# Performance work log

Hardware: AMD Instinct MI355X
Metric: run time of the kernel (lower is better)

## Reference

```python
import jax, jax.numpy as jnp
import numpy as np

B, M, H, D, C = 512, 40, 128, 64, 128


def setup_inputs() -> dict:
    key = jax.random.key(0)
    k1, k2, k3, k4 = jax.random.split(key, 4)
    x0 = jax.random.normal(k1, (B, M, D), dtype=jnp.float32)
    xk = jax.random.normal(k2, (B, H, D), dtype=jnp.float32)
    # Conv1d(kernel_size=1) weight [C, H*M, 1] squeezed to [C, H*M]; bias [C]
    W = jax.random.normal(k3, (C, H * M), dtype=jnp.float32) * 0.02
    b = jax.random.normal(k4, (C,), dtype=jnp.float32) * 0.02
    return {"x0": x0, "xk": xk, "W": W, "b": b}


def reference(x0, xk, W, b):
    # torch: outer[b, h*M+m, d] = xk[b,h,d] * x0[b,m,d]; out = conv1d(outer)
    # conv1d with kernel_size=1 is a channel contraction:
    #   out[b,c,d] = sum_{h,m} W[c, h*M+m] * xk[b,h,d] * x0[b,m,d] + b[c]
    Bsz, Hh, Dd = xk.shape
    Mm = x0.shape[1]
    Cc = W.shape[0]
    Wr = W.reshape(Cc, Hh, Mm)  # channel index is h*M + m -> [C, H, M]
    out = jnp.einsum('bhd,bmd,chm->bcd', xk, x0, Wr) + b[None, :, None]
    return out  # [B, C, D]
```

## Files before the change

kernel.cpp:

```cpp
#include <hip/hip_runtime.h>
#include <hip/hip_bf16.h>

typedef __attribute__((ext_vector_type(8))) short short8;
typedef __attribute__((ext_vector_type(4))) float f32x4;
typedef unsigned short u16;
typedef unsigned int u32;

#define NB 512
#define NM 40
#define NH 128
#define ND 64
#define NC 128
#define KTOT 5120

__device__ __forceinline__ u16 f2bf_rne(float f) {
    u32 u = __float_as_uint(f);
    u32 r = u + 0x7FFFu + ((u >> 16) & 1u);
    return (u16)(r >> 16);
}

__global__ void w3_kernel(const float* __restrict__ W, u16* __restrict__ W3) {
    __shared__ u16 kbuf[NH * 20];
    const int c = blockIdx.x >> 1, mh = blockIdx.x & 1;
    const float* src = W + (size_t)c * KTOT + mh * 20;
    for (int i = threadIdx.x; i < NH * 5; i += 256) {
        int h = i / 5, j4 = i % 5;
        float4 v = *(const float4*)(src + h * NM + j4 * 4);
        u16* kb = kbuf + h * 20 + j4 * 4;
        kb[0] = f2bf_rne(v.x); kb[1] = f2bf_rne(v.y);
        kb[2] = f2bf_rne(v.z); kb[3] = f2bf_rne(v.w);
    }
    __syncthreads();
    for (int i = threadIdx.x; i < 320; i += 256) {
        int mo = i >> 4, t = (i >> 2) & 3, q = i & 3;
        int n = (mh * 20 + mo) * 16 + t * 4 + q;
        union { short8 s8; u16 e[8]; } v;
#pragma unroll
        for (int j = 0; j < 8; ++j)
            v.e[j] = kbuf[(t * 32 + q * 8 + j) * 20 + mo];
        *(short8*)(W3 + ((size_t)n * 128 + c) * 8) = v.s8;
    }
}

__global__ void __launch_bounds__(512, 4) cin_main(
    const float* __restrict__ x0g, const float* __restrict__ xkg,
    const float* __restrict__ biasg, const u16* __restrict__ W3,
    float* __restrict__ out)
{
    __shared__ __align__(16) char smem[29824];
    short* xkT    = (short*)smem;
    float* x0s    = (float*)(smem + 18432);
    float* bias_s = (float*)(smem + 29312);

    const int tid = threadIdx.x;
    const int w = tid >> 6, L = tid & 63;
    const int q = L >> 4, l16 = L & 15;
    const int rh = w;
    const size_t b = blockIdx.x;

    const u16* Ap = W3 + q * 1024 + (size_t)(rh * 16 + l16) * 8;

    short8 aP[2];
    aP[0] = *(const short8*)(Ap + 0 * 4096);
    aP[1] = *(const short8*)(Ap + 1 * 4096);

    for (int i = tid; i < 2048; i += 512) {
        int h = i >> 4, d4 = (i & 15) << 2;
        float4 v = *(const float4*)(xkg + b * (NH * ND) + h * ND + d4);
        xkT[(d4 + 0) * 144 + h] = (short)f2bf_rne(v.x);
        xkT[(d4 + 1) * 144 + h] = (short)f2bf_rne(v.y);
        xkT[(d4 + 2) * 144 + h] = (short)f2bf_rne(v.z);
        xkT[(d4 + 3) * 144 + h] = (short)f2bf_rne(v.w);
    }
    for (int i = tid; i < 640; i += 512) {
        int m = i >> 4, d4 = (i & 15) << 2;
        *(f32x4*)(x0s + m * 68 + d4) =
            *(const f32x4*)(x0g + b * (NM * ND) + m * ND + d4);
    }
    if (tid < NC) bias_s[tid] = biasg[tid];
    __syncthreads();

    const short* Bp = xkT + (size_t)l16 * 144 + q * 8;
    short8 bR[4][4];
#pragma unroll
    for (int t = 0; t < 4; ++t)
#pragma unroll
        for (int n = 0; n < 4; ++n)
            bR[t][n] = *(const short8*)(Bp + n * (16 * 144) + t * 32);

    float s[4], sn[4];
#pragma unroll
    for (int n = 0; n < 4; ++n)
        s[n] = x0s[n * 16 + l16];

    f32x4 T[4] = {{0.f,0.f,0.f,0.f},{0.f,0.f,0.f,0.f},{0.f,0.f,0.f,0.f},{0.f,0.f,0.f,0.f}};
    f32x4 o[4] = {{0.f,0.f,0.f,0.f},{0.f,0.f,0.f,0.f},{0.f,0.f,0.f,0.f},{0.f,0.f,0.f,0.f}};

#pragma unroll 4
    for (int u = 0; u < 160; ++u) {
        const int t = u & 3;
        const short8 a = aP[u & 1];
        const int up = (u + 2 < 160) ? (u + 2) : 159;
        aP[u & 1] = *(const short8*)(Ap + (size_t)up * 4096);
        if (t == 0) {
            const int m = u >> 2;
#pragma unroll
            for (int n = 0; n < 4; ++n)
                sn[n] = (m < 39) ? x0s[(m + 1) * 68 + n * 16 + l16] : 0.f;
        }
        T[0] = __builtin_amdgcn_mfma_f32_16x16x32_bf16(a, bR[t][0], T[0], 0, 0, 0);
        T[1] = __builtin_amdgcn_mfma_f32_16x16x32_bf16(a, bR[t][1], T[1], 0, 0, 0);
        T[2] = __builtin_amdgcn_mfma_f32_16x16x32_bf16(a, bR[t][2], T[2], 0, 0, 0);
        T[3] = __builtin_amdgcn_mfma_f32_16x16x32_bf16(a, bR[t][3], T[3], 0, 0, 0);
        if (t == 3) {
#pragma unroll
            for (int n = 0; n < 4; ++n) {
                const float dd = s[n] - sn[n];
                o[n] += dd * T[n];
                s[n] = sn[n];
            }
        }
    }

    float* op = out + b * (NC * ND);
#pragma unroll
    for (int n = 0; n < 4; ++n) {
        const int d = n * 16 + l16;
#pragma unroll
        for (int rr = 0; rr < 4; ++rr) {
            const int c = rh * 16 + q * 4 + rr;
            op[c * ND + d] = o[n][rr] + bias_s[c];
        }
    }
}

extern "C" void kernel_launch(void* const* d_in, const int* in_sizes, int n_in,
                              void* d_out, int out_size, void* d_ws, size_t ws_size,
                              hipStream_t stream) {
    const float* x0 = (const float*)d_in[0];
    const float* xk = (const float*)d_in[1];
    const float* W  = (const float*)d_in[2];
    const float* bi = (const float*)d_in[3];
    float* out = (float*)d_out;

    u16* W3 = (u16*)d_ws;

    w3_kernel<<<NC * 2, 256, 0, stream>>>(W, W3);
    cin_main<<<NB, 512, 0, stream>>>(x0, xk, bi, W3, out);
}
```

Baseline: 116.4 us.

## Split output channels across blocks, split K across waves, stage W via LDS ring

```diff
diff --git a/kernel.cpp b/kernel.cpp
--- a/kernel.cpp
+++ b/kernel.cpp
@@ -17,6 +17,12 @@
     u32 u = __float_as_uint(f);
     u32 r = u + 0x7FFFu + ((u >> 16) & 1u);
     return (u16)(r >> 16);
+}
+
+__device__ __forceinline__ void gload16(const void* g, void* l) {
+    __builtin_amdgcn_global_load_lds(
+        (const __attribute__((address_space(1))) void*)g,
+        (__attribute__((address_space(3))) void*)l, 16, 0, 0);
 }
 
 __global__ void w3_kernel(const float* __restrict__ W, u16* __restrict__ W3) {
@@ -47,22 +53,30 @@
     const float* __restrict__ biasg, const u16* __restrict__ W3,
     float* __restrict__ out)
 {
-    __shared__ __align__(16) char smem[29824];
-    short* xkT    = (short*)smem;
-    float* x0s    = (float*)(smem + 18432);
-    float* bias_s = (float*)(smem + 29312);
+    __shared__ __align__(16) char smem[62592];
+    char*  ring   = smem;
+    float* red    = (float*)smem;
+    short* xkT    = (short*)(smem + 32768);
+    float* x0s    = (float*)(smem + 51200);
+    float* bias_s = (float*)(smem + 62080);
 
     const int tid = threadIdx.x;
     const int w = tid >> 6, L = tid & 63;
     const int q = L >> 4, l16 = L & 15;
-    const int rh = w;
-    const size_t b = blockIdx.x;
+    const int kh = w & 1;
+    const int rh = w >> 1;
+    const int ch = blockIdx.x & 1;
+    const size_t b = blockIdx.x >> 1;
 
-    const u16* Ap = W3 + q * 1024 + (size_t)(rh * 16 + l16) * 8;
+    const char* A0 = (const char*)W3
+        + (size_t)(kh * 16384 + q * 2048 + (ch * 64 + rh * 16 + l16) * 16);
+    char* ringw = ring + w * 4096;
 
-    short8 aP[2];
-    aP[0] = *(const short8*)(Ap + 0 * 4096);
-    aP[1] = *(const short8*)(Ap + 1 * 4096);
+    auto stage = [&](int ua, int slot) {
+        gload16(A0 + (size_t)(ua >> 1) * 32768 + (size_t)(ua & 1) * 8192,
+                ringw + slot * 1024 + L * 16);
+    };
+    stage(0, 0); stage(1, 1); stage(2, 2);
 
     for (int i = tid; i < 2048; i += 512) {
         int h = i >> 4, d4 = (i & 15) << 2;
@@ -80,13 +94,13 @@
     if (tid < NC) bias_s[tid] = biasg[tid];
     __syncthreads();
 
-    const short* Bp = xkT + (size_t)l16 * 144 + q * 8;
-    short8 bR[4][4];
+    const short* Bp = xkT + (size_t)l16 * 144 + kh * 64 + q * 8;
+    short8 bR[2][4];
 #pragma unroll
-    for (int t = 0; t < 4; ++t)
+    for (int th = 0; th < 2; ++th)
 #pragma unroll
         for (int n = 0; n < 4; ++n)
-            bR[t][n] = *(const short8*)(Bp + n * (16 * 144) + t * 32);
+            bR[th][n] = *(const short8*)(Bp + n * (16 * 144) + th * 32);
 
     float s[4], sn[4];
 #pragma unroll
@@ -97,22 +111,23 @@
     f32x4 o[4] = {{0.f,0.f,0.f,0.f},{0.f,0.f,0.f,0.f},{0.f,0.f,0.f,0.f},{0.f,0.f,0.f,0.f}};
 
 #pragma unroll 4
-    for (int u = 0; u < 160; ++u) {
-        const int t = u & 3;
-        const short8 a = aP[u & 1];
-        const int up = (u + 2 < 160) ? (u + 2) : 159;
-        aP[u & 1] = *(const short8*)(Ap + (size_t)up * 4096);
-        if (t == 0) {
-            const int m = u >> 2;
+    for (int u = 0; u < 80; ++u) {
+        const int th = u & 1;
+        const int un = u + 3;
+        stage((un < 80) ? un : 79, un & 3);
+        asm volatile("s_waitcnt vmcnt(3)" ::: "memory");
+        const short8 a = *(const short8*)(ringw + (u & 3) * 1024 + L * 16);
+        if (th == 0) {
+            const int m = u >> 1;
 #pragma unroll
             for (int n = 0; n < 4; ++n)
                 sn[n] = (m < 39) ? x0s[(m + 1) * 68 + n * 16 + l16] : 0.f;
         }
-        T[0] = __builtin_amdgcn_mfma_f32_16x16x32_bf16(a, bR[t][0], T[0], 0, 0, 0);
-        T[1] = __builtin_amdgcn_mfma_f32_16x16x32_bf16(a, bR[t][1], T[1], 0, 0, 0);
-        T[2] = __builtin_amdgcn_mfma_f32_16x16x32_bf16(a, bR[t][2], T[2], 0, 0, 0);
-        T[3] = __builtin_amdgcn_mfma_f32_16x16x32_bf16(a, bR[t][3], T[3], 0, 0, 0);
-        if (t == 3) {
+        T[0] = __builtin_amdgcn_mfma_f32_16x16x32_bf16(a, bR[th][0], T[0], 0, 0, 0);
+        T[1] = __builtin_amdgcn_mfma_f32_16x16x32_bf16(a, bR[th][1], T[1], 0, 0, 0);
+        T[2] = __builtin_amdgcn_mfma_f32_16x16x32_bf16(a, bR[th][2], T[2], 0, 0, 0);
+        T[3] = __builtin_amdgcn_mfma_f32_16x16x32_bf16(a, bR[th][3], T[3], 0, 0, 0);
+        if (th == 1) {
 #pragma unroll
             for (int n = 0; n < 4; ++n) {
                 const float dd = s[n] - sn[n];
@@ -122,14 +137,29 @@
         }
     }
 
-    float* op = out + b * (NC * ND);
+    asm volatile("s_waitcnt vmcnt(0)" ::: "memory");
+    __syncthreads();
+
+    float* myred = red + rh * 1280;
+    if (kh == 1) {
 #pragma unroll
-    for (int n = 0; n < 4; ++n) {
-        const int d = n * 16 + l16;
+        for (int n = 0; n < 4; ++n) {
+            int d = n * 16 + l16;
+            *(f32x4*)(myred + d * 20 + q * 4) = o[n];
+        }
+    }
+    __syncthreads();
+    if (kh == 0) {
+        float* op = out + b * (NC * ND);
 #pragma unroll
-        for (int rr = 0; rr < 4; ++rr) {
-            const int c = rh * 16 + q * 4 + rr;
-            op[c * ND + d] = o[n][rr] + bias_s[c];
+        for (int n = 0; n < 4; ++n) {
+            int d = n * 16 + l16;
+            f32x4 r = *(const f32x4*)(myred + d * 20 + q * 4);
+#pragma unroll
+            for (int rr = 0; rr < 4; ++rr) {
+                int c = ch * 64 + rh * 16 + q * 4 + rr;
+                op[c * ND + d] = o[n][rr] + r[rr] + bias_s[c];
+            }
         }
     }
 }
@@ -146,5 +176,5 @@
     u16* W3 = (u16*)d_ws;
 
     w3_kernel<<<NC * 2, 256, 0, stream>>>(W, W3);
-    cin_main<<<NB, 512, 0, stream>>>(x0, xk, bi, W3, out);
+    cin_main<<<NB * 2, 512, 0, stream>>>(x0, xk, bi, W3, out);
 }
```

Measured after the change: 126.2 us. 1.08x slower.

## Remap blocks to 4 batches × 32 channels, reusing W fragments across waves

Applied to the files above, without the earlier changes.

```diff
diff --git a/kernel.cpp b/kernel.cpp
--- a/kernel.cpp
+++ b/kernel.cpp
@@ -42,96 +42,103 @@
     }
 }
 
-__global__ void __launch_bounds__(512, 4) cin_main(
+__global__ void __launch_bounds__(256, 3) cin_main(
     const float* __restrict__ x0g, const float* __restrict__ xkg,
     const float* __restrict__ biasg, const u16* __restrict__ W3,
     float* __restrict__ out)
 {
-    __shared__ __align__(16) char smem[29824];
-    short* xkT    = (short*)smem;
-    float* x0s    = (float*)(smem + 18432);
-    float* bias_s = (float*)(smem + 29312);
+    __shared__ __align__(16) char smem[44032];
+    float* x0d    = (float*)smem;
+    float* bias_s = (float*)(smem + 43520);
 
     const int tid = threadIdx.x;
-    const int w = tid >> 6, L = tid & 63;
+    const int v = tid >> 6, L = tid & 63;
     const int q = L >> 4, l16 = L & 15;
-    const int rh = w;
-    const size_t b = blockIdx.x;
+    const int cq = blockIdx.x & 3;
+    const size_t b0 = 4 * (size_t)(blockIdx.x >> 2);
 
-    const u16* Ap = W3 + q * 1024 + (size_t)(rh * 16 + l16) * 8;
+    const char* A0 = (const char*)W3 + q * 2048 + cq * 512 + l16 * 16;
 
-    short8 aP[2];
-    aP[0] = *(const short8*)(Ap + 0 * 4096);
-    aP[1] = *(const short8*)(Ap + 1 * 4096);
+    short8 aP[2][2];
+    aP[0][0] = *(const short8*)(A0);
+    aP[0][1] = *(const short8*)(A0 + 256);
+    aP[1][0] = *(const short8*)(A0 + 8192);
+    aP[1][1] = *(const short8*)(A0 + 8192 + 256);
 
-    for (int i = tid; i < 2048; i += 512) {
-        int h = i >> 4, d4 = (i & 15) << 2;
-        float4 v = *(const float4*)(xkg + b * (NH * ND) + h * ND + d4);
-        xkT[(d4 + 0) * 144 + h] = (short)f2bf_rne(v.x);
-        xkT[(d4 + 1) * 144 + h] = (short)f2bf_rne(v.y);
-        xkT[(d4 + 2) * 144 + h] = (short)f2bf_rne(v.z);
-        xkT[(d4 + 3) * 144 + h] = (short)f2bf_rne(v.w);
-    }
-    for (int i = tid; i < 640; i += 512) {
-        int m = i >> 4, d4 = (i & 15) << 2;
-        *(f32x4*)(x0s + m * 68 + d4) =
-            *(const f32x4*)(x0g + b * (NM * ND) + m * ND + d4);
+    const float* xkb = xkg + (b0 + v) * (NH * ND);
+    short8 bR[4][4];
+#pragma unroll
+    for (int t = 0; t < 4; ++t)
+#pragma unroll
+        for (int n = 0; n < 4; ++n) {
+            union { short8 s8; u16 e[8]; } tmp;
+#pragma unroll
+            for (int j = 0; j < 8; ++j)
+                tmp.e[j] = f2bf_rne(xkb[(t * 32 + q * 8 + j) * ND + n * 16 + l16]);
+            bR[t][n] = tmp.s8;
+        }
+
+    for (int i = tid; i < 2560; i += 256) {
+        int b2 = i / 640, rem = i % 640;
+        int m = rem >> 4, d4 = (rem & 15) << 2;
+        const float* xp = x0g + (b0 + b2) * (NM * ND) + m * ND + d4;
+        float4 cur = *(const float4*)xp;
+        float4 nxt = make_float4(0.f, 0.f, 0.f, 0.f);
+        if (m < 39) nxt = *(const float4*)(xp + ND);
+        f32x4 dv;
+        dv[0] = cur.x - nxt.x; dv[1] = cur.y - nxt.y;
+        dv[2] = cur.z - nxt.z; dv[3] = cur.w - nxt.w;
+        *(f32x4*)(x0d + b2 * 2720 + m * 68 + d4) = dv;
     }
     if (tid < NC) bias_s[tid] = biasg[tid];
     __syncthreads();
 
-    const short* Bp = xkT + (size_t)l16 * 144 + q * 8;
-    short8 bR[4][4];
-#pragma unroll
-    for (int t = 0; t < 4; ++t)
-#pragma unroll
-        for (int n = 0; n < 4; ++n)
-            bR[t][n] = *(const short8*)(Bp + n * (16 * 144) + t * 32);
+    const float* dd0 = x0d + v * 2720 + (size_t)l16;
 
-    float s[4], sn[4];
-#pragma unroll
-    for (int n = 0; n < 4; ++n)
-        s[n] = x0s[n * 16 + l16];
-
-    f32x4 T[4] = {{0.f,0.f,0.f,0.f},{0.f,0.f,0.f,0.f},{0.f,0.f,0.f,0.f},{0.f,0.f,0.f,0.f}};
-    f32x4 o[4] = {{0.f,0.f,0.f,0.f},{0.f,0.f,0.f,0.f},{0.f,0.f,0.f,0.f},{0.f,0.f,0.f,0.f}};
+    f32x4 T[2][4] = {};
+    f32x4 o[2][4] = {};
 
 #pragma unroll 4
     for (int u = 0; u < 160; ++u) {
         const int t = u & 3;
-        const short8 a = aP[u & 1];
+        const short8 a0 = aP[u & 1][0];
+        const short8 a1 = aP[u & 1][1];
         const int up = (u + 2 < 160) ? (u + 2) : 159;
-        aP[u & 1] = *(const short8*)(Ap + (size_t)up * 4096);
-        if (t == 0) {
+        const char* p = A0 + (size_t)(up >> 2) * 32768 + (size_t)(up & 3) * 8192;
+        aP[u & 1][0] = *(const short8*)p;
+        aP[u & 1][1] = *(const short8*)(p + 256);
+        T[0][0] = __builtin_amdgcn_mfma_f32_16x16x32_bf16(a0, bR[t][0], T[0][0], 0, 0, 0);
+        T[0][1] = __builtin_amdgcn_mfma_f32_16x16x32_bf16(a0, bR[t][1], T[0][1], 0, 0, 0);
+        T[0][2] = __builtin_amdgcn_mfma_f32_16x16x32_bf16(a0, bR[t][2], T[0][2], 0, 0, 0);
+        T[0][3] = __builtin_amdgcn_mfma_f32_16x16x32_bf16(a0, bR[t][3], T[0][3], 0, 0, 0);
+        T[1][0] = __builtin_amdgcn_mfma_f32_16x16x32_bf16(a1, bR[t][0], T[1][0], 0, 0, 0);
+        T[1][1] = __builtin_amdgcn_mfma_f32_16x16x32_bf16(a1, bR[t][1], T[1][1], 0, 0, 0);
+        T[1][2] = __builtin_amdgcn_mfma_f32_16x16x32_bf16(a1, bR[t][2], T[1][2], 0, 0, 0);
+        T[1][3] = __builtin_amdgcn_mfma_f32_16x16x32_bf16(a1, bR[t][3], T[1][3], 0, 0, 0);
+        if (t == 3) {
             const int m = u >> 2;
 #pragma unroll
-            for (int n = 0; n < 4; ++n)
-                sn[n] = (m < 39) ? x0s[(m + 1) * 68 + n * 16 + l16] : 0.f;
-        }
-        T[0] = __builtin_amdgcn_mfma_f32_16x16x32_bf16(a, bR[t][0], T[0], 0, 0, 0);
-        T[1] = __builtin_amdgcn_mfma_f32_16x16x32_bf16(a, bR[t][1], T[1], 0, 0, 0);
-        T[2] = __builtin_amdgcn_mfma_f32_16x16x32_bf16(a, bR[t][2], T[2], 0, 0, 0);
-        T[3] = __builtin_amdgcn_mfma_f32_16x16x32_bf16(a, bR[t][3], T[3], 0, 0, 0);
-        if (t == 3) {
-#pragma unroll
             for (int n = 0; n < 4; ++n) {
-                const float dd = s[n] - sn[n];
-                o[n] += dd * T[n];
-                s[n] = sn[n];
+                const float dd = dd0[m * 68 + n * 16];
+                o[0][n] += dd * T[0][n];
+                o[1][n] += dd * T[1][n];
             }
         }
+        if ((u & 31) == 31) __builtin_amdgcn_s_barrier();
     }
 
-    float* op = out + b * (NC * ND);
+    float* op = out + (b0 + v) * (NC * ND);
 #pragma unroll
-    for (int n = 0; n < 4; ++n) {
-        const int d = n * 16 + l16;
+    for (int mt = 0; mt < 2; ++mt)
 #pragma unroll
-        for (int rr = 0; rr < 4; ++rr) {
-            const int c = rh * 16 + q * 4 + rr;
-            op[c * ND + d] = o[n][rr] + bias_s[c];
+        for (int n = 0; n < 4; ++n) {
+            const int d = n * 16 + l16;
+#pragma unroll
+            for (int rr = 0; rr < 4; ++rr) {
+                const int c = cq * 32 + mt * 16 + q * 4 + rr;
+                op[c * ND + d] = o[mt][n][rr] + bias_s[c];
+            }
         }
-    }
 }
 
 extern "C" void kernel_launch(void* const* d_in, const int* in_sizes, int n_in,
@@ -146,5 +153,5 @@
     u16* W3 = (u16*)d_ws;
 
     w3_kernel<<<NC * 2, 256, 0, stream>>>(W, W3);
-    cin_main<<<NB, 512, 0, stream>>>(x0, xk, bi, W3, out);
+    cin_main<<<NB / 4 * 4, 256, 0, stream>>>(x0, xk, bi, W3, out);
 }
```

After: 130.3 us. 11.9% more time.
